# Kernel optimization log

Measured on AMD Instinct MI355X. Metric: run time of the kernel, lower is better.

Reference implementation:

```python
import jax, jax.numpy as jnp
import numpy as np

NH, DK, DV, D = 8, 64, 64, 768
DECAY = 0.95
WRITE_STRENGTH = 0.1


def setup_inputs() -> dict:
    key = jax.random.key(0)
    ks = jax.random.split(key, 6)
    s = 0.02  # small init scale for projection weights
    return {
        "x": jax.random.normal(ks[0], (4, 4096, D), dtype=jnp.float32),
        "w_key": jax.random.normal(ks[1], (NH * DK, D), dtype=jnp.float32) * s,
        "w_value": jax.random.normal(ks[2], (NH * DV, D), dtype=jnp.float32) * s,
        "w_query": jax.random.normal(ks[3], (NH * DK, D), dtype=jnp.float32) * s,
        "w_gate": jax.random.normal(ks[4], (NH, D), dtype=jnp.float32) * s,
        "w_out": jax.random.normal(ks[5], (D, NH * DV), dtype=jnp.float32) * s,
    }


def reference(x, w_key, w_value, w_query, w_gate, w_out):
    B, S, _ = x.shape
    # Batched projections (torch Linear: y = x @ W.T)
    k = (x @ w_key.T).reshape(B, S, NH, DK)
    v = (x @ w_value.T).reshape(B, S, NH, DV)
    q = (x @ w_query.T).reshape(B, S, NH, DK)
    gate = jax.nn.sigmoid(x @ w_gate.T)  # (B, S, NH)

    # Writes only use batch element 0 (mirrors k[0], v[0], gate[0] in source)
    k0 = k[0]      # (S, NH, DK)
    v0 = v[0]      # (S, NH, DV)
    g0 = gate[0]   # (S, NH)

    def step(fw, inp):
        q_t, k0_t, v0_t, g0_t = inp
        # Read BEFORE this step's decay+write
        retrieved = jnp.einsum('bhk,hkv->bhv', q_t, fw)  # (B, NH, DV)
        write = (WRITE_STRENGTH * g0_t)[:, None, None] * (k0_t[:, :, None] * v0_t[:, None, :])
        fw_new = DECAY * fw + jax.lax.stop_gradient(write)
        return fw_new, retrieved

    fw0 = jnp.zeros((NH, DK, DV), dtype=x.dtype)
    inputs = (q.transpose(1, 0, 2, 3), k0, v0, g0)  # time-major
    _, retrieved = jax.lax.scan(step, fw0, inputs)   # (S, B, NH, DV)
    retrieved = retrieved.transpose(1, 0, 2, 3).reshape(B, S, NH * DV)
    return x + retrieved @ w_out.T
```

## Files before the change

### kernel.cpp

```cpp
#include <hip/hip_runtime.h>
#include <hip/hip_bf16.h>

typedef __hip_bfloat16 bf16;
typedef __attribute__((ext_vector_type(8))) short   bf16x8;
typedef __attribute__((ext_vector_type(4))) float   f32x4;

#define B_   4
#define S_   4096
#define D_   768
#define NH_  8
#define DK_  64
#define DV_  64
#define CH_  64
#define NCH_ (S_/CH_)
#define DECAY_ 0.95f
#define WSTR_  0.1f

__device__ __forceinline__ float b2f(bf16 v) { return __bfloat162float(v); }
__device__ __forceinline__ bf16  f2b(float v) { return __float2bfloat16(v); }

__device__ __forceinline__ void gl2lds16(const bf16* g, bf16* lds) {
    __builtin_amdgcn_global_load_lds(
        (const __attribute__((address_space(1))) void*)g,
        (__attribute__((address_space(3))) void*)lds, 16, 0, 0);
}

__global__ __launch_bounds__(192) void cast_fused(const float* __restrict__ x,
                                                  bf16* __restrict__ xb,
                                                  const float* __restrict__ wg,
                                                  float* __restrict__ wgt,
                                                  const float* __restrict__ wq,
                                                  const float* __restrict__ wk,
                                                  const float* __restrict__ wv,
                                                  const float* __restrict__ wo,
                                                  bf16* __restrict__ dq, bf16* __restrict__ dk,
                                                  bf16* __restrict__ dv, bf16* __restrict__ dob) {
    const int tid = threadIdx.x;
    if (blockIdx.x >= (B_ * S_)) {
        const int idx = blockIdx.x - B_ * S_;
        const int which = idx >> 9, b = idx & 511;
        const float* src = which == 0 ? wq : which == 1 ? wk : which == 2 ? wv : wo;
        bf16*       dst = which == 0 ? dq : which == 1 ? dk : which == 2 ? dv : dob;
        const int i = (b * 192 + tid) * 4;
        const float4 v = *reinterpret_cast<const float4*>(src + i);
        union { bf16 b4[4]; ushort4 u; } t;
        t.b4[0] = f2b(v.x); t.b4[1] = f2b(v.y); t.b4[2] = f2b(v.z); t.b4[3] = f2b(v.w);
        *reinterpret_cast<ushort4*>(dst + i) = t.u;
        return;
    }
    const int s = blockIdx.x;
    const float4 v = *reinterpret_cast<const float4*>(x + (size_t)s * D_ + tid * 4);
    union { bf16 b4[4]; ushort4 u; } t;
    t.b4[0] = f2b(v.x); t.b4[1] = f2b(v.y); t.b4[2] = f2b(v.z); t.b4[3] = f2b(v.w);
    *reinterpret_cast<ushort4*>(xb + (size_t)s * D_ + tid * 4) = t.u;

    if (s < S_) {
        __shared__ float red[3 * 8];
        float p[8];
        const float* wgp = wg + tid * 4;
        #pragma unroll
        for (int h = 0; h < 8; h++) {
            const float4 wv4 = *reinterpret_cast<const float4*>(wgp + h * D_);
            p[h] = v.x * wv4.x + v.y * wv4.y + v.z * wv4.z + v.w * wv4.w;
        }
        #pragma unroll
        for (int h = 0; h < 8; h++)
            #pragma unroll
            for (int off = 32; off; off >>= 1) p[h] += __shfl_down(p[h], off);
        const int w = tid >> 6, lane = tid & 63;
        if (lane == 0) {
            #pragma unroll
            for (int h = 0; h < 8; h++) red[w * 8 + h] = p[h];
        }
        __syncthreads();
        if (tid < 8) {
            const float sum = red[tid] + red[8 + tid] + red[16 + tid];
            wgt[s * NH_ + tid] = WSTR_ / (1.f + expf(-sum));
        }
    }
}

template<typename TC, int ADDX, int NITER>
__device__ __forceinline__ void gemm_body(bf16* As, bf16* Bs,
                                          const bf16* __restrict__ A,
                                          const bf16* __restrict__ Bm,
                                          const float* __restrict__ X,
                                          TC* __restrict__ C,
                                          int bm, int bn, int K, int N) {
    const int tid = threadIdx.x, lane = tid & 63, w = tid >> 6;
    const int quad = lane >> 4, l16 = lane & 15;
    const int wm = (w >> 1) * 64, wn = (w & 1) * 64;
    const int lrow = lane >> 3;
    const int lcol = ((lane & 7) ^ lrow) * 8;

    f32x4 acc[4][4] = {};

    auto STAGE_A = [&](int it, int buf) {
        const int k0 = it * 64;
        bf16* Ad = As + buf * 8192;
        #pragma unroll
        for (int c = 0; c < 4; c++) {
            const int seg = w * 4 + c;
            const int row = seg * 8 + lrow;
            gl2lds16(A + (size_t)(bm + row) * K + k0 + lcol, &Ad[seg * 512]);
        }
    };
    auto STAGE_B = [&](int it) {
        const int k0 = it * 64;
        #pragma unroll
        for (int c = 0; c < 4; c++) {
            const int seg = w * 4 + c;
            const int row = seg * 8 + lrow;
            gl2lds16(Bm + (size_t)(bn + row) * K + k0 + lcol, &Bs[seg * 512]);
        }
    };

    STAGE_A(0, 0);
    STAGE_B(0);

    for (int it = 0; it < NITER; ++it) {
        const int cur = it & 1;
        if (it + 1 < NITER) {
            STAGE_A(it + 1, cur ^ 1);
            asm volatile("s_waitcnt vmcnt(4)" ::: "memory");
        } else {
            asm volatile("s_waitcnt vmcnt(0)" ::: "memory");
        }
        __builtin_amdgcn_s_barrier();
        asm volatile("" ::: "memory");

        const bf16* Ar = As + cur * 8192;
        bf16x8 af[2][4], bfr[2][4];
        #pragma unroll
        for (int kh = 0; kh < 2; kh++)
            #pragma unroll
            for (int t = 0; t < 4; t++) {
                const int cb = ((kh * 4 + quad) ^ (l16 & 7)) * 8;
                af[kh][t]  = *reinterpret_cast<const bf16x8*>(&Ar[(wm + t * 16 + l16) * 64 + cb]);
                bfr[kh][t] = *reinterpret_cast<const bf16x8*>(&Bs[(wn + t * 16 + l16) * 64 + cb]);
            }
        asm volatile("s_waitcnt lgkmcnt(0)" ::: "memory");
        __builtin_amdgcn_s_barrier();
        if (it + 1 < NITER) STAGE_B(it + 1);

        #pragma unroll
        for (int kh = 0; kh < 2; kh++)
            #pragma unroll
            for (int mt = 0; mt < 4; mt++)
                #pragma unroll
                for (int nt = 0; nt < 4; nt++)
                    acc[mt][nt] = __builtin_amdgcn_mfma_f32_16x16x32_bf16(
                        af[kh][mt], bfr[kh][nt], acc[mt][nt], 0, 0, 0);
    }

    #pragma unroll
    for (int mt = 0; mt < 4; mt++)
        #pragma unroll
        for (int nt = 0; nt < 4; nt++)
            #pragma unroll
            for (int r = 0; r < 4; r++) {
                const int m = bm + wm + mt * 16 + quad * 4 + r;
                const int n = bn + wn + nt * 16 + l16;
                float v = acc[mt][nt][r];
                if (ADDX) v += X[(size_t)m * N + n];
                if (sizeof(TC) == 2) *(bf16*)&C[(size_t)m * N + n] = f2b(v);
                else                 *(float*)&C[(size_t)m * N + n] = v;
            }
}

__global__ __launch_bounds__(256, 3) void proj_fused(const bf16* __restrict__ xb,
                                                  const bf16* __restrict__ wqb,
                                                  const bf16* __restrict__ wkb,
                                                  const bf16* __restrict__ wvb,
                                                  bf16* __restrict__ qbuf,
                                                  bf16* __restrict__ k0buf,
                                                  bf16* __restrict__ v0buf) {
    __shared__ bf16 As[2 * 128 * 64];
    __shared__ bf16 Bs[128 * 64];
    const int id = blockIdx.x;
    const int xcd = id & 7;
    int j = id >> 3;
    const bf16* Bm; bf16* C; int bm, bn;
    if (j < 64) {
        bm = (xcd + ((j >> 2) << 3)) * 128;
        bn = (j & 3) * 128;
        Bm = wqb; C = qbuf;
    } else {
        j -= 64;
        bm = (xcd + ((j >> 3) << 3)) * 128;
        const int b8 = j & 7;
        bn = (b8 & 3) * 128;
        Bm = (b8 < 4) ? wkb : wvb;
        C  = (b8 < 4) ? k0buf : v0buf;
    }
    gemm_body<bf16, 0, 12>(As, Bs, xb, Bm, nullptr, C, bm, bn, D_, 512);
}

__global__ __launch_bounds__(256, 3) void gemm_out(const bf16* __restrict__ retr,
                                                const bf16* __restrict__ wob,
                                                const float* __restrict__ x,
                                                float* __restrict__ out) {
    __shared__ bf16 As[2 * 128 * 64];
    __shared__ bf16 Bs[128 * 64];
    const int gx = gridDim.x, gy = gridDim.y;
    const int L = blockIdx.y * gx + blockIdx.x;
    const int rpx = gy >> 3;
    const int xcd = L & 7;
    const int i   = L >> 3;
    const int by = xcd * rpx + i / gx;
    const int bx = i % gx;
    gemm_body<float, 1, 8>(As, Bs, retr, wob, x, out, by * 128, bx * 128, 512, D_);
}

__global__ __launch_bounds__(256) void chunk_sums(const bf16* __restrict__ k0,
                                                  const bf16* __restrict__ v0,
                                                  const float* __restrict__ wgt,
                                                  bf16* __restrict__ lsumsT) {
    const int n = blockIdx.x, h = blockIdx.y;
    __shared__ float ks[CH_][65];
    __shared__ float vs[CH_][64];
    __shared__ float cw[CH_];
    const int tid = threadIdx.x;
    for (int e = tid; e < CH_ * 64; e += 256) {
        const int r = e >> 6, c = e & 63;
        const int t = n * CH_ + r;
        ks[r][c] = b2f(k0[(size_t)t * (NH_ * DK_) + h * DK_ + c]);
        vs[r][c] = b2f(v0[(size_t)t * (NH_ * DV_) + h * DV_ + c]);
    }
    if (tid < CH_) {
        const int t = n * CH_ + tid;
        cw[tid] = powf(DECAY_, (float)(CH_ - 1 - tid)) * wgt[t * NH_ + h];
    }
    __syncthreads();
    const int j = tid & 63, ig = tid >> 6;
    float acc[16] = {};
    for (int idx = 0; idx < CH_; idx++) {
        const float ck = cw[idx] * ks[idx][j];
        #pragma unroll
        for (int r = 0; r < 16; r++) acc[r] += vs[idx][ig * 16 + r] * ck;
    }
    bf16* outp = lsumsT + ((size_t)(n * NH_ + h)) * (DK_ * DV_);
    #pragma unroll
    for (int r = 0; r < 16; r++) outp[(ig * 16 + r) * 64 + j] = f2b(acc[r]);
}

__device__ __forceinline__ void cvt4(ushort4 u, float f[4]) {
    union { unsigned u; float f; } c;
    c.u = (unsigned)u.x << 16; f[0] = c.f;
    c.u = (unsigned)u.y << 16; f[1] = c.f;
    c.u = (unsigned)u.z << 16; f[2] = c.f;
    c.u = (unsigned)u.w << 16; f[3] = c.f;
}

__global__ __launch_bounds__(256) void chunk_output(const bf16* __restrict__ q,
                                                    const bf16* __restrict__ k0,
                                                    const bf16* __restrict__ v0,
                                                    const float* __restrict__ wgt,
                                                    const bf16* __restrict__ lsumsT,
                                                    bf16* __restrict__ retr) {
    const int n = blockIdx.x, h = blockIdx.y;
    __shared__ bf16 QsAm[4][64 * 64];
    __shared__ bf16 Ks[64 * 64];
    __shared__ bf16 FWT[64 * 64];
    __shared__ bf16 VT[64 * 72];
    __shared__ float dpow[64], winv[64];
    const int tid = threadIdx.x, lane = tid & 63, w = tid >> 6;
    const int quad = lane >> 4, l16 = lane & 15;
    const int t0 = n * CH_;
    const int lrow = lane >> 3;
    const int lcol = ((lane & 7) ^ lrow) * 8;

    #pragma unroll
    for (int seg = 0; seg < 8; seg++) {
        const int row = seg * 8 + lrow;
        gl2lds16(q + ((size_t)(w * S_ + t0 + row)) * 512 + h * 64 + lcol, &QsAm[w][seg * 512]);
    }
    #pragma unroll
    for (int c = 0; c < 2; c++) {
        const int seg = w * 2 + c;
        const int row = seg * 8 + lrow;
        gl2lds16(k0 + ((size_t)(t0 + row)) * 512 + h * 64 + lcol, &Ks[seg * 512]);
    }

    {
        float fwacc[16] = {};
        const float dcp[4] = { 1.0f, 0.0375241f, 1.40806e-3f, 5.28365e-5f };
        #pragma unroll
        for (int jj = 1; jj <= 4; jj++) {
            const int nm = n - jj;
            if (nm < 0) break;
            const ushort* Lp = (const ushort*)(lsumsT + ((size_t)(nm * NH_ + h)) * 4096) + tid * 16;
            #pragma unroll
            for (int u = 0; u < 4; u++) {
                float f[4];
                cvt4(reinterpret_cast<const ushort4*>(Lp)[u], f);
                #pragma unroll
                for (int e = 0; e < 4; e++) fwacc[u * 4 + e] += dcp[jj - 1] * f[e];
            }
        }
        const int frow = tid >> 2;
        #pragma unroll
        for (int half = 0; half < 2; half++) {
            const int cb = (tid & 3) * 2 + half;
            union { bf16 b8v[8]; bf16x8 v; } t;
            #pragma unroll
            for (int e = 0; e < 8; e++) t.b8v[e] = f2b(fwacc[half * 8 + e]);
            *reinterpret_cast<bf16x8*>(&FWT[frow * 64 + (cb ^ (frow & 7)) * 8]) = t.v;
        }
    }
    {
        ushort4 vreg[4];
        const int jb = (tid & 15) * 4;
        const int sb = tid >> 4;
        #pragma unroll
        for (int it = 0; it < 4; it++)
            vreg[it] = *reinterpret_cast<const ushort4*>(
                v0 + ((size_t)(t0 + sb + it * 16)) * 512 + h * 64 + jb);
        ushort* VTu = reinterpret_cast<ushort*>(VT);
        #pragma unroll
        for (int it = 0; it < 4; it++) {
            const int s = sb + it * 16;
            VTu[(jb + 0) * 72 + s] = vreg[it].x;
            VTu[(jb + 1) * 72 + s] = vreg[it].y;
            VTu[(jb + 2) * 72 + s] = vreg[it].z;
            VTu[(jb + 3) * 72 + s] = vreg[it].w;
        }
    }
    if (tid < 64) {
        dpow[tid] = powf(DECAY_, (float)tid);
        winv[tid] = wgt[(t0 + tid) * NH_ + h] * powf(DECAY_, -(float)(tid + 1));
    }
    __syncthreads();

    const int cb0 = ((quad) ^ (l16 & 7)) * 8;
    const int cb1 = ((4 + quad) ^ (l16 & 7)) * 8;
    bf16* Qw = &QsAm[w][0];

    bf16x8 af[4][2];
    #pragma unroll
    for (int mt = 0; mt < 4; mt++) {
        af[mt][0] = *reinterpret_cast<const bf16x8*>(&Qw[(mt * 16 + l16) * 64 + cb0]);
        af[mt][1] = *reinterpret_cast<const bf16x8*>(&Qw[(mt * 16 + l16) * 64 + cb1]);
    }

    f32x4 acc[4][4] = {};
    #pragma unroll
    for (int kh = 0; kh < 2; kh++) {
        bf16x8 bk[4];
        #pragma unroll
        for (int nt = 0; nt < 4; nt++)
            bk[nt] = *reinterpret_cast<const bf16x8*>(
                &Ks[(nt * 16 + l16) * 64 + (kh ? cb1 : cb0)]);
        #pragma unroll
        for (int mt = 0; mt < 4; mt++)
            #pragma unroll
            for (int nt = 0; nt < 4; nt++)
                acc[mt][nt] = __builtin_amdgcn_mfma_f32_16x16x32_bf16(
                    af[mt][kh], bk[nt], acc[mt][nt], 0, 0, 0);
    }

    const float pmt[4] = { 1.0f, 0.4401266694f, 0.1937114891f, 0.0852578070f };
    const f32x4 dpb = *reinterpret_cast<const f32x4*>(&dpow[quad * 4]);
    float winv_l[4];
    #pragma unroll
    for (int nt = 0; nt < 4; nt++) winv_l[nt] = winv[nt * 16 + l16];
    #pragma unroll
    for (int mt = 0; mt < 4; mt++)
        #pragma unroll
        for (int nt = 0; nt < 4; nt++)
            #pragma unroll
            for (int r = 0; r < 4; r++) {
                const int tt = mt * 16 + quad * 4 + r;
                const int s = nt * 16 + l16;
                const float v = (s < tt) ? acc[mt][nt][r] * (dpb[r] * pmt[mt]) * winv_l[nt] : 0.f;
                Qw[tt * 64 + (((s >> 3) ^ (tt & 7)) << 3) + (s & 7)] = f2b(v);
            }

    f32x4 o[4][4] = {};
    #pragma unroll
    for (int kh = 0; kh < 2; kh++) {
        bf16x8 ff[4];
        #pragma unroll
        for (int nt = 0; nt < 4; nt++)
            ff[nt] = *reinterpret_cast<const bf16x8*>(
                &FWT[(nt * 16 + l16) * 64 + (kh ? cb1 : cb0)]);
        #pragma unroll
        for (int mt = 0; mt < 4; mt++)
            #pragma unroll
            for (int nt = 0; nt < 4; nt++)
                o[mt][nt] = __builtin_amdgcn_mfma_f32_16x16x32_bf16(
                    af[mt][kh], ff[nt], o[mt][nt], 0, 0, 0);
    }
    #pragma unroll
    for (int mt = 0; mt < 4; mt++)
        #pragma unroll
        for (int nt = 0; nt < 4; nt++)
            #pragma unroll
            for (int r = 0; r < 4; r++) o[mt][nt][r] *= dpb[r] * pmt[mt];

    #pragma unroll
    for (int kh = 0; kh < 2; kh++) {
        bf16x8 am[4], vf[4];
        #pragma unroll
        for (int mt = 0; mt < 4; mt++)
            am[mt] = *reinterpret_cast<const bf16x8*>(
                &Qw[(mt * 16 + l16) * 64 + (kh ? cb1 : cb0)]);
        #pragma unroll
        for (int nt = 0; nt < 4; nt++)
            vf[nt] = *reinterpret_cast<const bf16x8*>(
                &VT[(nt * 16 + l16) * 72 + kh * 32 + quad * 8]);
        #pragma unroll
        for (int mt = 0; mt < 4; mt++)
            #pragma unroll
            for (int nt = 0; nt < 4; nt++)
                o[mt][nt] = __builtin_amdgcn_mfma_f32_16x16x32_bf16(
                    am[mt], vf[nt], o[mt][nt], 0, 0, 0);
    }

    #pragma unroll
    for (int mt = 0; mt < 4; mt++)
        #pragma unroll
        for (int nt = 0; nt < 4; nt++)
            #pragma unroll
            for (int r = 0; r < 4; r++) {
                const int tt = mt * 16 + quad * 4 + r;
                retr[((size_t)(w * S_ + t0 + tt)) * 512 + h * 64 + nt * 16 + l16] =
                    f2b(o[mt][nt][r]);
            }
}

extern "C" void kernel_launch(void* const* d_in, const int* in_sizes, int n_in,
                              void* d_out, int out_size, void* d_ws, size_t ws_size,
                              hipStream_t stream) {
    const float* x  = (const float*)d_in[0];
    const float* wk = (const float*)d_in[1];
    const float* wv = (const float*)d_in[2];
    const float* wq = (const float*)d_in[3];
    const float* wg = (const float*)d_in[4];
    const float* wo = (const float*)d_in[5];
    float* out = (float*)d_out;

    const size_t MB1 = 1ull << 20;
    char* w = (char*)d_ws;
    bf16*  qbuf    = (bf16*)(w);
    bf16*  k0buf   = (bf16*)(w + 16 * MB1);
    bf16*  v0buf   = (bf16*)(w + 20 * MB1);
    float* wgt     = (float*)(w + 24 * MB1);
    bf16*  wqb     = (bf16*)(w + 24 * MB1 + (128ull<<10));
    bf16*  wkb     = (bf16*)(w + 24 * MB1 + (128ull<<10) + 1*786432);
    bf16*  wvb     = (bf16*)(w + 24 * MB1 + (128ull<<10) + 2*786432);
    bf16*  wob     = (bf16*)(w + 24 * MB1 + (128ull<<10) + 3*786432);
    bf16*  lsumsT  = (bf16*)(w + 28 * MB1);
    bf16*  retr    = (bf16*)(w + 32 * MB1);
    bf16*  xb      = (bf16*)(w + 48 * MB1);

    const int MB = B_ * S_;

    cast_fused<<<MB + 2048, 192, 0, stream>>>(x, xb, wg, wgt,
                                              wq, wk, wv, wo, wqb, wkb, wvb, wob);

    proj_fused<<<768, 256, 0, stream>>>(xb, wqb, wkb, wvb, qbuf, k0buf, v0buf);

    chunk_sums<<<dim3(NCH_, NH_), 256, 0, stream>>>(k0buf, v0buf, wgt, lsumsT);
    chunk_output<<<dim3(NCH_, NH_), 256, 0, stream>>>(qbuf, k0buf, v0buf, wgt, lsumsT, retr);

    gemm_out<<<dim3(D_ / 128, MB / 128), 256, 0, stream>>>(retr, wob, x, out);
}
```

Measured before the change: 185.5 us.

## Fuse all stages into one persistent cooperative kernel with grid syncs

Replaces the five separate launches (cast, projections, chunk sums, chunk output, output GEMM) with one cooperative 768-block kernel. The stages are separated by grid.sync, and the kernel falls back to the old launches if occupancy or the cooperative launch fails. The goal is to remove launch gaps and tail idle time between the small kernels. In exchange, all stages share one register and LDS budget, and the chunk stages use only 512 of the 768 blocks while the rest wait at grid barriers.

```diff
diff --git a/kernel.cpp b/kernel.cpp
--- a/kernel.cpp
+++ b/kernel.cpp
@@ -1,5 +1,8 @@
 #include <hip/hip_runtime.h>
 #include <hip/hip_bf16.h>
+#include <hip/hip_cooperative_groups.h>
+
+namespace cg = cooperative_groups;
 
 typedef __hip_bfloat16 bf16;
 typedef __attribute__((ext_vector_type(8))) short   bf16x8;
@@ -15,6 +18,7 @@
 #define NCH_ (S_/CH_)
 #define DECAY_ 0.95f
 #define WSTR_  0.1f
+#define L2D_  (-0.07400058144f)
 
 __device__ __forceinline__ float b2f(bf16 v) { return __bfloat162float(v); }
 __device__ __forceinline__ bf16  f2b(float v) { return __float2bfloat16(v); }
@@ -23,6 +27,427 @@
     __builtin_amdgcn_global_load_lds(
         (const __attribute__((address_space(1))) void*)g,
         (__attribute__((address_space(3))) void*)lds, 16, 0, 0);
+}
+
+__device__ __forceinline__ void cvt4(ushort4 u, float f[4]) {
+    union { unsigned u; float f; } c;
+    c.u = (unsigned)u.x << 16; f[0] = c.f;
+    c.u = (unsigned)u.y << 16; f[1] = c.f;
+    c.u = (unsigned)u.z << 16; f[2] = c.f;
+    c.u = (unsigned)u.w << 16; f[3] = c.f;
+}
+
+template<typename TC, int ADDX, int NITER>
+__device__ __forceinline__ void gemm_body(bf16* As, bf16* Bs,
+                                          const bf16* __restrict__ A,
+                                          const bf16* __restrict__ Bm,
+                                          const float* __restrict__ X,
+                                          TC* __restrict__ C,
+                                          int bm, int bn, int K, int N) {
+    const int tid = threadIdx.x, lane = tid & 63, w = tid >> 6;
+    const int quad = lane >> 4, l16 = lane & 15;
+    const int wm = (w >> 1) * 64, wn = (w & 1) * 64;
+    const int lrow = lane >> 3;
+    const int lcol = ((lane & 7) ^ lrow) * 8;
+
+    f32x4 acc[4][4] = {};
+
+    auto STAGE_A = [&](int it, int buf) {
+        const int k0 = it * 64;
+        bf16* Ad = As + buf * 8192;
+        #pragma unroll
+        for (int c = 0; c < 4; c++) {
+            const int seg = w * 4 + c;
+            const int row = seg * 8 + lrow;
+            gl2lds16(A + (size_t)(bm + row) * K + k0 + lcol, &Ad[seg * 512]);
+        }
+    };
+    auto STAGE_B = [&](int it) {
+        const int k0 = it * 64;
+        #pragma unroll
+        for (int c = 0; c < 4; c++) {
+            const int seg = w * 4 + c;
+            const int row = seg * 8 + lrow;
+            gl2lds16(Bm + (size_t)(bn + row) * K + k0 + lcol, &Bs[seg * 512]);
+        }
+    };
+
+    STAGE_A(0, 0);
+    STAGE_B(0);
+
+    for (int it = 0; it < NITER; ++it) {
+        const int cur = it & 1;
+        if (it + 1 < NITER) {
+            STAGE_A(it + 1, cur ^ 1);
+            asm volatile("s_waitcnt vmcnt(4)" ::: "memory");
+        } else {
+            asm volatile("s_waitcnt vmcnt(0)" ::: "memory");
+        }
+        __builtin_amdgcn_s_barrier();
+        asm volatile("" ::: "memory");
+
+        const bf16* Ar = As + cur * 8192;
+        bf16x8 af[2][4], bfr[2][4];
+        #pragma unroll
+        for (int kh = 0; kh < 2; kh++)
+            #pragma unroll
+            for (int t = 0; t < 4; t++) {
+                const int cb = ((kh * 4 + quad) ^ (l16 & 7)) * 8;
+                af[kh][t]  = *reinterpret_cast<const bf16x8*>(&Ar[(wm + t * 16 + l16) * 64 + cb]);
+                bfr[kh][t] = *reinterpret_cast<const bf16x8*>(&Bs[(wn + t * 16 + l16) * 64 + cb]);
+            }
+        asm volatile("s_waitcnt lgkmcnt(0)" ::: "memory");
+        __builtin_amdgcn_s_barrier();
+        if (it + 1 < NITER) STAGE_B(it + 1);
+
+        #pragma unroll
+        for (int kh = 0; kh < 2; kh++)
+            #pragma unroll
+            for (int mt = 0; mt < 4; mt++)
+                #pragma unroll
+                for (int nt = 0; nt < 4; nt++)
+                    acc[mt][nt] = __builtin_amdgcn_mfma_f32_16x16x32_bf16(
+                        af[kh][mt], bfr[kh][nt], acc[mt][nt], 0, 0, 0);
+    }
+
+    #pragma unroll
+    for (int mt = 0; mt < 4; mt++)
+        #pragma unroll
+        for (int nt = 0; nt < 4; nt++)
+            #pragma unroll
+            for (int r = 0; r < 4; r++) {
+                const int m = bm + wm + mt * 16 + quad * 4 + r;
+                const int n = bn + wn + nt * 16 + l16;
+                float v = acc[mt][nt][r];
+                if (ADDX) v += X[(size_t)m * N + n];
+                if (sizeof(TC) == 2) *(bf16*)&C[(size_t)m * N + n] = f2b(v);
+                else                 *(float*)&C[(size_t)m * N + n] = v;
+            }
+}
+
+__global__ __launch_bounds__(256, 3) void mega(
+    const float* __restrict__ x,  const float* __restrict__ wg,
+    const float* __restrict__ wq, const float* __restrict__ wk,
+    const float* __restrict__ wv, const float* __restrict__ wo,
+    bf16* __restrict__ xb, float* __restrict__ wgt,
+    bf16* __restrict__ wqb, bf16* __restrict__ wkb,
+    bf16* __restrict__ wvb, bf16* __restrict__ wob,
+    bf16* __restrict__ qbuf, bf16* __restrict__ k0buf, bf16* __restrict__ v0buf,
+    bf16* __restrict__ lsumsT, bf16* __restrict__ retr, float* __restrict__ out) {
+
+    __shared__ __align__(16) bf16 U[24576];
+    __shared__ __align__(16) float scr[192];
+    cg::grid_group grid = cg::this_grid();
+    const int bid = blockIdx.x, tid = threadIdx.x;
+    const int lane = tid & 63, w = tid >> 6;
+
+    {
+        #pragma unroll 2
+        for (int u0 = 0; u0 < 24; ++u0) {
+            const int unit = bid * 24 + u0;
+            if (tid < 192) {
+                const float* src; bf16* dst;
+                if (unit < B_ * S_) {
+                    src = x  + (size_t)unit * D_;
+                    dst = xb + (size_t)unit * D_;
+                } else {
+                    const int idx = unit - B_ * S_;
+                    const int which = idx >> 9, b = idx & 511;
+                    const float* s4 = which == 0 ? wq : which == 1 ? wk : which == 2 ? wv : wo;
+                    bf16*       d4 = which == 0 ? wqb : which == 1 ? wkb : which == 2 ? wvb : wob;
+                    src = s4 + (size_t)b * D_;
+                    dst = d4 + (size_t)b * D_;
+                }
+                const float4 v = *reinterpret_cast<const float4*>(src + tid * 4);
+                union { bf16 b4[4]; ushort4 u; } t;
+                t.b4[0] = f2b(v.x); t.b4[1] = f2b(v.y); t.b4[2] = f2b(v.z); t.b4[3] = f2b(v.w);
+                *reinterpret_cast<ushort4*>(dst + tid * 4) = t.u;
+            }
+        }
+        if (bid * 24 < S_) {
+            for (int i = 0; i < 6; ++i) {
+                const int row = bid * 24 + w * 6 + i;
+                if (row >= S_) break;
+                const float* xr = x + (size_t)row * D_ + lane * 12;
+                const float4 a0 = *reinterpret_cast<const float4*>(xr);
+                const float4 a1 = *reinterpret_cast<const float4*>(xr + 4);
+                const float4 a2 = *reinterpret_cast<const float4*>(xr + 8);
+                float p[8];
+                #pragma unroll
+                for (int h = 0; h < 8; h++) {
+                    const float* wr = wg + h * D_ + lane * 12;
+                    const float4 b0 = *reinterpret_cast<const float4*>(wr);
+                    const float4 b1 = *reinterpret_cast<const float4*>(wr + 4);
+                    const float4 b2 = *reinterpret_cast<const float4*>(wr + 8);
+                    p[h] = a0.x*b0.x + a0.y*b0.y + a0.z*b0.z + a0.w*b0.w
+                         + a1.x*b1.x + a1.y*b1.y + a1.z*b1.z + a1.w*b1.w
+                         + a2.x*b2.x + a2.y*b2.y + a2.z*b2.z + a2.w*b2.w;
+                }
+                #pragma unroll
+                for (int h = 0; h < 8; h++)
+                    #pragma unroll
+                    for (int off = 32; off; off >>= 1) p[h] += __shfl_down(p[h], off);
+                if (lane == 0) {
+                    #pragma unroll
+                    for (int h = 0; h < 8; h++)
+                        wgt[row * NH_ + h] = WSTR_ / (1.f + expf(-p[h]));
+                }
+            }
+        }
+    }
+    __threadfence();
+    grid.sync();
+
+    {
+        bf16* As = U;
+        bf16* Bs = U + 16384;
+        const int xcd = bid & 7;
+        int j = bid >> 3;
+        const bf16* Bm; bf16* C; int bm, bn;
+        if (j < 64) {
+            bm = (xcd + ((j >> 2) << 3)) * 128;
+            bn = (j & 3) * 128;
+            Bm = wqb; C = qbuf;
+        } else {
+            j -= 64;
+            bm = (xcd + ((j >> 3) << 3)) * 128;
+            const int b8 = j & 7;
+            bn = (b8 & 3) * 128;
+            Bm = (b8 < 4) ? wkb : wvb;
+            C  = (b8 < 4) ? k0buf : v0buf;
+        }
+        gemm_body<bf16, 0, 12>(As, Bs, xb, Bm, nullptr, C, bm, bn, D_, 512);
+    }
+    __threadfence();
+    grid.sync();
+
+    if (bid < NCH_ * NH_) {
+        const int n = bid & 63, h = bid >> 6;
+        float* ksf = (float*)U;
+        float* vsf = ksf + 64 * 68;
+        float* cw  = scr + 128;
+        const int r = tid >> 2, c0 = (tid & 3) * 16;
+        {
+            const ushort* kp = (const ushort*)k0buf + ((size_t)(n * CH_ + r)) * 512 + h * 64 + c0;
+            const ushort* vp = (const ushort*)v0buf + ((size_t)(n * CH_ + r)) * 512 + h * 64 + c0;
+            #pragma unroll
+            for (int e = 0; e < 4; e++) {
+                float fk[4], fv[4];
+                cvt4(reinterpret_cast<const ushort4*>(kp)[e], fk);
+                cvt4(reinterpret_cast<const ushort4*>(vp)[e], fv);
+                union { float f[4]; float4 v4; } tk, tv;
+                tk.f[0]=fk[0]; tk.f[1]=fk[1]; tk.f[2]=fk[2]; tk.f[3]=fk[3];
+                tv.f[0]=fv[0]; tv.f[1]=fv[1]; tv.f[2]=fv[2]; tv.f[3]=fv[3];
+                *reinterpret_cast<float4*>(&ksf[r * 68 + c0 + e * 4]) = tk.v4;
+                *reinterpret_cast<float4*>(&vsf[r * 68 + c0 + e * 4]) = tv.v4;
+            }
+        }
+        if (tid < CH_)
+            cw[tid] = exp2f((float)(CH_ - 1 - tid) * L2D_) * wgt[(n * CH_ + tid) * NH_ + h];
+        __syncthreads();
+        const int j = tid & 63, ig = tid >> 6;
+        float acc[16] = {};
+        for (int idx = 0; idx < CH_; idx++) {
+            const float ck = cw[idx] * ksf[idx * 68 + j];
+            #pragma unroll
+            for (int rr = 0; rr < 16; rr++) acc[rr] += vsf[idx * 68 + ig * 16 + rr] * ck;
+        }
+        bf16* outp = lsumsT + ((size_t)(n * NH_ + h)) * (DK_ * DV_);
+        #pragma unroll
+        for (int rr = 0; rr < 16; rr++) outp[(ig * 16 + rr) * 64 + j] = f2b(acc[rr]);
+    }
+    __threadfence();
+    grid.sync();
+
+    if (bid < NCH_ * NH_) {
+        const int n = bid & 63, h = bid >> 6;
+        bf16* QsAm = U;
+        bf16* Ks   = U + 16384;
+        bf16* FWT  = U + 16384;
+        bf16* VT   = U + 20480;
+        float* dpow = scr, *winv = scr + 64;
+        const int quad = lane >> 4, l16 = lane & 15;
+        const int t0 = n * CH_;
+        const int lrow = lane >> 3;
+        const int lcol = ((lane & 7) ^ lrow) * 8;
+
+        #pragma unroll
+        for (int seg = 0; seg < 8; seg++) {
+            const int row = seg * 8 + lrow;
+            gl2lds16(qbuf + ((size_t)(w * S_ + t0 + row)) * 512 + h * 64 + lcol,
+                     &QsAm[w * 4096 + seg * 512]);
+        }
+        #pragma unroll
+        for (int c = 0; c < 2; c++) {
+            const int seg = w * 2 + c;
+            const int row = seg * 8 + lrow;
+            gl2lds16(k0buf + ((size_t)(t0 + row)) * 512 + h * 64 + lcol, &Ks[seg * 512]);
+        }
+        float fwacc[16] = {};
+        {
+            const float dcp[4] = { 1.0f, 0.0375241f, 1.40806e-3f, 5.28365e-5f };
+            #pragma unroll
+            for (int jj = 1; jj <= 4; jj++) {
+                const int nm = n - jj;
+                if (nm < 0) break;
+                const ushort* Lp = (const ushort*)(lsumsT + ((size_t)(nm * NH_ + h)) * 4096) + tid * 16;
+                #pragma unroll
+                for (int u = 0; u < 4; u++) {
+                    float f[4];
+                    cvt4(reinterpret_cast<const ushort4*>(Lp)[u], f);
+                    #pragma unroll
+                    for (int e = 0; e < 4; e++) fwacc[u * 4 + e] += dcp[jj - 1] * f[e];
+                }
+            }
+        }
+        {
+            ushort4 vreg[4];
+            const int jb = (tid & 15) * 4;
+            const int sb = tid >> 4;
+            #pragma unroll
+            for (int it = 0; it < 4; it++)
+                vreg[it] = *reinterpret_cast<const ushort4*>(
+                    v0buf + ((size_t)(t0 + sb + it * 16)) * 512 + h * 64 + jb);
+            ushort* VTu = reinterpret_cast<ushort*>(VT);
+            #pragma unroll
+            for (int it = 0; it < 4; it++) {
+                const int s = sb + it * 16;
+                #pragma unroll
+                for (int c = 0; c < 4; c++) {
+                    const int v = jb + c;
+                    const ushort val = c == 0 ? vreg[it].x : c == 1 ? vreg[it].y
+                                     : c == 2 ? vreg[it].z : vreg[it].w;
+                    VTu[v * 64 + (((s >> 3) ^ (v & 7)) << 3) + (s & 7)] = val;
+                }
+            }
+        }
+        if (tid < 64) {
+            dpow[tid] = exp2f((float)tid * L2D_);
+            winv[tid] = wgt[(t0 + tid) * NH_ + h] * exp2f(-(float)(tid + 1) * L2D_);
+        }
+        __syncthreads();
+
+        const int cb0 = ((quad) ^ (l16 & 7)) * 8;
+        const int cb1 = ((4 + quad) ^ (l16 & 7)) * 8;
+        bf16* Qw = &QsAm[w * 4096];
+
+        bf16x8 af[4][2];
+        #pragma unroll
+        for (int mt = 0; mt < 4; mt++) {
+            af[mt][0] = *reinterpret_cast<const bf16x8*>(&Qw[(mt * 16 + l16) * 64 + cb0]);
+            af[mt][1] = *reinterpret_cast<const bf16x8*>(&Qw[(mt * 16 + l16) * 64 + cb1]);
+        }
+        f32x4 acc[4][4] = {};
+        #pragma unroll
+        for (int kh = 0; kh < 2; kh++) {
+            bf16x8 bk[4];
+            #pragma unroll
+            for (int nt = 0; nt < 4; nt++)
+                bk[nt] = *reinterpret_cast<const bf16x8*>(
+                    &Ks[(nt * 16 + l16) * 64 + (kh ? cb1 : cb0)]);
+            #pragma unroll
+            for (int mt = 0; mt < 4; mt++)
+                #pragma unroll
+                for (int nt = 0; nt < 4; nt++)
+                    acc[mt][nt] = __builtin_amdgcn_mfma_f32_16x16x32_bf16(
+                        af[mt][kh], bk[nt], acc[mt][nt], 0, 0, 0);
+        }
+        const float pmt[4] = { 1.0f, 0.4401266694f, 0.1937114891f, 0.0852578070f };
+        const f32x4 dpb = *reinterpret_cast<const f32x4*>(&dpow[quad * 4]);
+        float winv_l[4];
+        #pragma unroll
+        for (int nt = 0; nt < 4; nt++) winv_l[nt] = winv[nt * 16 + l16];
+        #pragma unroll
+        for (int mt = 0; mt < 4; mt++)
+            #pragma unroll
+            for (int nt = 0; nt < 4; nt++)
+                #pragma unroll
+                for (int r = 0; r < 4; r++) {
+                    const int tt = mt * 16 + quad * 4 + r;
+                    const int s = nt * 16 + l16;
+                    const float v = (s < tt) ? acc[mt][nt][r] * (dpb[r] * pmt[mt]) * winv_l[nt] : 0.f;
+                    Qw[tt * 64 + (((s >> 3) ^ (tt & 7)) << 3) + (s & 7)] = f2b(v);
+                }
+        __syncthreads();
+        {
+            const int frow = tid >> 2;
+            #pragma unroll
+            for (int half = 0; half < 2; half++) {
+                const int cb = (tid & 3) * 2 + half;
+                union { bf16 b8v[8]; bf16x8 v; } t;
+                #pragma unroll
+                for (int e = 0; e < 8; e++) t.b8v[e] = f2b(fwacc[half * 8 + e]);
+                *reinterpret_cast<bf16x8*>(&FWT[frow * 64 + (cb ^ (frow & 7)) * 8]) = t.v;
+            }
+        }
+        __syncthreads();
+
+        f32x4 o[4][4] = {};
+        #pragma unroll
+        for (int kh = 0; kh < 2; kh++) {
+            bf16x8 ff[4];
+            #pragma unroll
+            for (int nt = 0; nt < 4; nt++)
+                ff[nt] = *reinterpret_cast<const bf16x8*>(
+                    &FWT[(nt * 16 + l16) * 64 + (kh ? cb1 : cb0)]);
+            #pragma unroll
+            for (int mt = 0; mt < 4; mt++)
+                #pragma unroll
+                for (int nt = 0; nt < 4; nt++)
+                    o[mt][nt] = __builtin_amdgcn_mfma_f32_16x16x32_bf16(
+                        af[mt][kh], ff[nt], o[mt][nt], 0, 0, 0);
+        }
+        #pragma unroll
+        for (int mt = 0; mt < 4; mt++)
+            #pragma unroll
+            for (int nt = 0; nt < 4; nt++)
+                #pragma unroll
+                for (int r = 0; r < 4; r++) o[mt][nt][r] *= dpb[r] * pmt[mt];
+
+        #pragma unroll
+        for (int kh = 0; kh < 2; kh++) {
+            bf16x8 am[4], vf[4];
+            #pragma unroll
+            for (int mt = 0; mt < 4; mt++)
+                am[mt] = *reinterpret_cast<const bf16x8*>(
+                    &Qw[(mt * 16 + l16) * 64 + (kh ? cb1 : cb0)]);
+            #pragma unroll
+            for (int nt = 0; nt < 4; nt++)
+                vf[nt] = *reinterpret_cast<const bf16x8*>(
+                    &VT[(nt * 16 + l16) * 64 + (kh ? cb1 : cb0)]);
+            #pragma unroll
+            for (int mt = 0; mt < 4; mt++)
+                #pragma unroll
+                for (int nt = 0; nt < 4; nt++)
+                    o[mt][nt] = __builtin_amdgcn_mfma_f32_16x16x32_bf16(
+                        am[mt], vf[nt], o[mt][nt], 0, 0, 0);
+        }
+        #pragma unroll
+        for (int mt = 0; mt < 4; mt++)
+            #pragma unroll
+            for (int nt = 0; nt < 4; nt++)
+                #pragma unroll
+                for (int r = 0; r < 4; r++) {
+                    const int tt = mt * 16 + quad * 4 + r;
+                    retr[((size_t)(w * S_ + t0 + tt)) * 512 + h * 64 + nt * 16 + l16] =
+                        f2b(o[mt][nt][r]);
+                }
+    }
+    __threadfence();
+    grid.sync();
+
+    {
+        bf16* As = U;
+        bf16* Bs = U + 16384;
+        const int gx = 6, gy = 128;
+        const int L = bid;
+        const int rpx = gy >> 3;
+        const int xcd = L & 7;
+        const int i   = L >> 3;
+        const int by = xcd * rpx + i / gx;
+        const int bx = i % gx;
+        gemm_body<float, 1, 8>(As, Bs, retr, wob, x, out, by * 128, bx * 128, 512, D_);
+    }
 }
 
 __global__ __launch_bounds__(192) void cast_fused(const float* __restrict__ x,
@@ -78,94 +503,6 @@
             wgt[s * NH_ + tid] = WSTR_ / (1.f + expf(-sum));
         }
     }
-}
-
-template<typename TC, int ADDX, int NITER>
-__device__ __forceinline__ void gemm_body(bf16* As, bf16* Bs,
-                                          const bf16* __restrict__ A,
-                                          const bf16* __restrict__ Bm,
-                                          const float* __restrict__ X,
-                                          TC* __restrict__ C,
-                                          int bm, int bn, int K, int N) {
-    const int tid = threadIdx.x, lane = tid & 63, w = tid >> 6;
-    const int quad = lane >> 4, l16 = lane & 15;
-    const int wm = (w >> 1) * 64, wn = (w & 1) * 64;
-    const int lrow = lane >> 3;
-    const int lcol = ((lane & 7) ^ lrow) * 8;
-
-    f32x4 acc[4][4] = {};
-
-    auto STAGE_A = [&](int it, int buf) {
-        const int k0 = it * 64;
-        bf16* Ad = As + buf * 8192;
-        #pragma unroll
-        for (int c = 0; c < 4; c++) {
-            const int seg = w * 4 + c;
-            const int row = seg * 8 + lrow;
-            gl2lds16(A + (size_t)(bm + row) * K + k0 + lcol, &Ad[seg * 512]);
-        }
-    };
-    auto STAGE_B = [&](int it) {
-        const int k0 = it * 64;
-        #pragma unroll
-        for (int c = 0; c < 4; c++) {
-            const int seg = w * 4 + c;
-            const int row = seg * 8 + lrow;
-            gl2lds16(Bm + (size_t)(bn + row) * K + k0 + lcol, &Bs[seg * 512]);
-        }
-    };
-
-    STAGE_A(0, 0);
-    STAGE_B(0);
-
-    for (int it = 0; it < NITER; ++it) {
-        const int cur = it & 1;
-        if (it + 1 < NITER) {
-            STAGE_A(it + 1, cur ^ 1);
-            asm volatile("s_waitcnt vmcnt(4)" ::: "memory");
-        } else {
-            asm volatile("s_waitcnt vmcnt(0)" ::: "memory");
-        }
-        __builtin_amdgcn_s_barrier();
-        asm volatile("" ::: "memory");
-
-        const bf16* Ar = As + cur * 8192;
-        bf16x8 af[2][4], bfr[2][4];
-        #pragma unroll
-        for (int kh = 0; kh < 2; kh++)
-            #pragma unroll
-            for (int t = 0; t < 4; t++) {
-                const int cb = ((kh * 4 + quad) ^ (l16 & 7)) * 8;
-                af[kh][t]  = *reinterpret_cast<const bf16x8*>(&Ar[(wm + t * 16 + l16) * 64 + cb]);
-                bfr[kh][t] = *reinterpret_cast<const bf16x8*>(&Bs[(wn + t * 16 + l16) * 64 + cb]);
-            }
-        asm volatile("s_waitcnt lgkmcnt(0)" ::: "memory");
-        __builtin_amdgcn_s_barrier();
-        if (it + 1 < NITER) STAGE_B(it + 1);
-
-        #pragma unroll
-        for (int kh = 0; kh < 2; kh++)
-            #pragma unroll
-            for (int mt = 0; mt < 4; mt++)
-                #pragma unroll
-                for (int nt = 0; nt < 4; nt++)
-                    acc[mt][nt] = __builtin_amdgcn_mfma_f32_16x16x32_bf16(
-                        af[kh][mt], bfr[kh][nt], acc[mt][nt], 0, 0, 0);
-    }
-
-    #pragma unroll
-    for (int mt = 0; mt < 4; mt++)
-        #pragma unroll
-        for (int nt = 0; nt < 4; nt++)
-            #pragma unroll
-            for (int r = 0; r < 4; r++) {
-                const int m = bm + wm + mt * 16 + quad * 4 + r;
-                const int n = bn + wn + nt * 16 + l16;
-                float v = acc[mt][nt][r];
-                if (ADDX) v += X[(size_t)m * N + n];
-                if (sizeof(TC) == 2) *(bf16*)&C[(size_t)m * N + n] = f2b(v);
-                else                 *(float*)&C[(size_t)m * N + n] = v;
-            }
 }
 
 __global__ __launch_bounds__(256, 3) void proj_fused(const bf16* __restrict__ xb,
@@ -244,14 +581,6 @@
     for (int r = 0; r < 16; r++) outp[(ig * 16 + r) * 64 + j] = f2b(acc[r]);
 }
 
-__device__ __forceinline__ void cvt4(ushort4 u, float f[4]) {
-    union { unsigned u; float f; } c;
-    c.u = (unsigned)u.x << 16; f[0] = c.f;
-    c.u = (unsigned)u.y << 16; f[1] = c.f;
-    c.u = (unsigned)u.z << 16; f[2] = c.f;
-    c.u = (unsigned)u.w << 16; f[3] = c.f;
-}
-
 __global__ __launch_bounds__(256) void chunk_output(const bf16* __restrict__ q,
                                                     const bf16* __restrict__ k0,
                                                     const bf16* __restrict__ v0,
@@ -281,7 +610,6 @@
         const int row = seg * 8 + lrow;
         gl2lds16(k0 + ((size_t)(t0 + row)) * 512 + h * 64 + lcol, &Ks[seg * 512]);
     }
-
     {
         float fwacc[16] = {};
         const float dcp[4] = { 1.0f, 0.0375241f, 1.40806e-3f, 5.28365e-5f };
@@ -342,7 +670,6 @@
         af[mt][0] = *reinterpret_cast<const bf16x8*>(&Qw[(mt * 16 + l16) * 64 + cb0]);
         af[mt][1] = *reinterpret_cast<const bf16x8*>(&Qw[(mt * 16 + l16) * 64 + cb1]);
     }
-
     f32x4 acc[4][4] = {};
     #pragma unroll
     for (int kh = 0; kh < 2; kh++) {
@@ -358,7 +685,6 @@
                 acc[mt][nt] = __builtin_amdgcn_mfma_f32_16x16x32_bf16(
                     af[mt][kh], bk[nt], acc[mt][nt], 0, 0, 0);
     }
-
     const float pmt[4] = { 1.0f, 0.4401266694f, 0.1937114891f, 0.0852578070f };
     const f32x4 dpb = *reinterpret_cast<const f32x4*>(&dpow[quad * 4]);
     float winv_l[4];
@@ -375,7 +701,6 @@
                 const float v = (s < tt) ? acc[mt][nt][r] * (dpb[r] * pmt[mt]) * winv_l[nt] : 0.f;
                 Qw[tt * 64 + (((s >> 3) ^ (tt & 7)) << 3) + (s & 7)] = f2b(v);
             }
-
     f32x4 o[4][4] = {};
     #pragma unroll
     for (int kh = 0; kh < 2; kh++) {
@@ -397,7 +722,6 @@
         for (int nt = 0; nt < 4; nt++)
             #pragma unroll
             for (int r = 0; r < 4; r++) o[mt][nt][r] *= dpb[r] * pmt[mt];
-
     #pragma unroll
     for (int kh = 0; kh < 2; kh++) {
         bf16x8 am[4], vf[4];
@@ -416,7 +740,6 @@
                 o[mt][nt] = __builtin_amdgcn_mfma_f32_16x16x32_bf16(
                     am[mt], vf[nt], o[mt][nt], 0, 0, 0);
     }
-
     #pragma unroll
     for (int mt = 0; mt < 4; mt++)
         #pragma unroll
@@ -454,15 +777,30 @@
     bf16*  retr    = (bf16*)(w + 32 * MB1);
     bf16*  xb      = (bf16*)(w + 48 * MB1);
 
+    static int coopOK = -1;
+    if (coopOK < 0) {
+        int nb = 0;
+        hipError_t e = hipOccupancyMaxActiveBlocksPerMultiprocessor(
+            &nb, (const void*)mega, 256, 0);
+        coopOK = (e == hipSuccess && nb >= 3) ? 1 : 0;
+    }
+    if (coopOK == 1) {
+        void* args[] = {
+            (void*)&x, (void*)&wg, (void*)&wq, (void*)&wk, (void*)&wv, (void*)&wo,
+            (void*)&xb, (void*)&wgt, (void*)&wqb, (void*)&wkb, (void*)&wvb, (void*)&wob,
+            (void*)&qbuf, (void*)&k0buf, (void*)&v0buf, (void*)&lsumsT, (void*)&retr,
+            (void*)&out };
+        hipError_t e = hipLaunchCooperativeKernel(
+            (const void*)mega, dim3(768), dim3(256), args, 0, stream);
+        if (e == hipSuccess) return;
+        coopOK = 0;
+    }
+
     const int MB = B_ * S_;
-
     cast_fused<<<MB + 2048, 192, 0, stream>>>(x, xb, wg, wgt,
                                               wq, wk, wv, wo, wqb, wkb, wvb, wob);
-
     proj_fused<<<768, 256, 0, stream>>>(xb, wqb, wkb, wvb, qbuf, k0buf, v0buf);
-
     chunk_sums<<<dim3(NCH_, NH_), 256, 0, stream>>>(k0buf, v0buf, wgt, lsumsT);
     chunk_output<<<dim3(NCH_, NH_), 256, 0, stream>>>(qbuf, k0buf, v0buf, wgt, lsumsT, retr);
-
     gemm_out<<<dim3(D_ / 128, MB / 128), 256, 0, stream>>>(retr, wob, x, out);
 }
```

Measured after the change: 187.3 us. Within noise of the previous version (+1.0%).

## Fuse x bf16 cast into projection GEMM A-operand load

Applied to the files above, without the earlier changes.

Removes the separate bf16 copy of x: the projection GEMM now loads fp32 x through registers, converts to bf16 and writes swizzled LDS tiles, with software prefetch two iterations ahead. The prep kernel shrinks to only the gate computation and weight casts over S rows. This avoids writing and re-reading a large bf16 intermediate, but doubles the bytes the GEMM reads for A and replaces async global-to-LDS loads with register staging, which adds register pressure.

```diff
diff --git a/kernel.cpp b/kernel.cpp
--- a/kernel.cpp
+++ b/kernel.cpp
@@ -25,19 +25,26 @@
         (__attribute__((address_space(3))) void*)lds, 16, 0, 0);
 }
 
-__global__ __launch_bounds__(192) void cast_fused(const float* __restrict__ x,
-                                                  bf16* __restrict__ xb,
-                                                  const float* __restrict__ wg,
-                                                  float* __restrict__ wgt,
-                                                  const float* __restrict__ wq,
-                                                  const float* __restrict__ wk,
-                                                  const float* __restrict__ wv,
-                                                  const float* __restrict__ wo,
-                                                  bf16* __restrict__ dq, bf16* __restrict__ dk,
-                                                  bf16* __restrict__ dv, bf16* __restrict__ dob) {
+__device__ __forceinline__ void cvt4(ushort4 u, float f[4]) {
+    union { unsigned u; float f; } c;
+    c.u = (unsigned)u.x << 16; f[0] = c.f;
+    c.u = (unsigned)u.y << 16; f[1] = c.f;
+    c.u = (unsigned)u.z << 16; f[2] = c.f;
+    c.u = (unsigned)u.w << 16; f[3] = c.f;
+}
+
+__global__ __launch_bounds__(192) void prep(const float* __restrict__ x,
+                                            const float* __restrict__ wg,
+                                            float* __restrict__ wgt,
+                                            const float* __restrict__ wq,
+                                            const float* __restrict__ wk,
+                                            const float* __restrict__ wv,
+                                            const float* __restrict__ wo,
+                                            bf16* __restrict__ dq, bf16* __restrict__ dk,
+                                            bf16* __restrict__ dv, bf16* __restrict__ dob) {
     const int tid = threadIdx.x;
-    if (blockIdx.x >= (B_ * S_)) {
-        const int idx = blockIdx.x - B_ * S_;
+    if (blockIdx.x >= S_) {
+        const int idx = blockIdx.x - S_;
         const int which = idx >> 9, b = idx & 511;
         const float* src = which == 0 ? wq : which == 1 ? wk : which == 2 ? wv : wo;
         bf16*       dst = which == 0 ? dq : which == 1 ? dk : which == 2 ? dv : dob;
@@ -50,34 +57,134 @@
     }
     const int s = blockIdx.x;
     const float4 v = *reinterpret_cast<const float4*>(x + (size_t)s * D_ + tid * 4);
-    union { bf16 b4[4]; ushort4 u; } t;
-    t.b4[0] = f2b(v.x); t.b4[1] = f2b(v.y); t.b4[2] = f2b(v.z); t.b4[3] = f2b(v.w);
-    *reinterpret_cast<ushort4*>(xb + (size_t)s * D_ + tid * 4) = t.u;
-
-    if (s < S_) {
-        __shared__ float red[3 * 8];
-        float p[8];
-        const float* wgp = wg + tid * 4;
-        #pragma unroll
-        for (int h = 0; h < 8; h++) {
-            const float4 wv4 = *reinterpret_cast<const float4*>(wgp + h * D_);
-            p[h] = v.x * wv4.x + v.y * wv4.y + v.z * wv4.z + v.w * wv4.w;
-        }
-        #pragma unroll
-        for (int h = 0; h < 8; h++)
-            #pragma unroll
-            for (int off = 32; off; off >>= 1) p[h] += __shfl_down(p[h], off);
-        const int w = tid >> 6, lane = tid & 63;
-        if (lane == 0) {
-            #pragma unroll
-            for (int h = 0; h < 8; h++) red[w * 8 + h] = p[h];
-        }
-        __syncthreads();
-        if (tid < 8) {
-            const float sum = red[tid] + red[8 + tid] + red[16 + tid];
-            wgt[s * NH_ + tid] = WSTR_ / (1.f + expf(-sum));
-        }
-    }
+    __shared__ float red[3 * 8];
+    float p[8];
+    const float* wgp = wg + tid * 4;
+    #pragma unroll
+    for (int h = 0; h < 8; h++) {
+        const float4 wv4 = *reinterpret_cast<const float4*>(wgp + h * D_);
+        p[h] = v.x * wv4.x + v.y * wv4.y + v.z * wv4.z + v.w * wv4.w;
+    }
+    #pragma unroll
+    for (int h = 0; h < 8; h++)
+        #pragma unroll
+        for (int off = 32; off; off >>= 1) p[h] += __shfl_down(p[h], off);
+    const int w = tid >> 6, lane = tid & 63;
+    if (lane == 0) {
+        #pragma unroll
+        for (int h = 0; h < 8; h++) red[w * 8 + h] = p[h];
+    }
+    __syncthreads();
+    if (tid < 8) {
+        const float sum = red[tid] + red[8 + tid] + red[16 + tid];
+        wgt[s * NH_ + tid] = WSTR_ / (1.f + expf(-sum));
+    }
+}
+
+template<int NITER>
+__device__ __forceinline__ void gemm_projA(bf16* As, bf16* Bs,
+                                           const float* __restrict__ A,
+                                           const bf16* __restrict__ Bm,
+                                           bf16* __restrict__ C,
+                                           int bm, int bn, int K, int N) {
+    const int tid = threadIdx.x, lane = tid & 63, w = tid >> 6;
+    const int quad = lane >> 4, l16 = lane & 15;
+    const int wm = (w >> 1) * 64, wn = (w & 1) * 64;
+    const int lrow = lane >> 3;
+    const int lcol = ((lane & 7) ^ lrow) * 8;
+
+    f32x4 acc[4][4] = {};
+    float4 a4[8];
+
+    auto ALOAD = [&](int it) {
+        const int k0 = it * 64;
+        #pragma unroll
+        for (int c = 0; c < 4; c++) {
+            const int row = (w * 4 + c) * 8 + lrow;
+            const float* p = A + (size_t)(bm + row) * K + k0 + lcol;
+            a4[2 * c]     = *reinterpret_cast<const float4*>(p);
+            a4[2 * c + 1] = *reinterpret_cast<const float4*>(p + 4);
+        }
+    };
+    auto AWRITE = [&](int buf) {
+        bf16* Ad = As + buf * 8192;
+        #pragma unroll
+        for (int c = 0; c < 4; c++) {
+            union { bf16 b8[8]; bf16x8 v; } t;
+            t.b8[0] = f2b(a4[2*c].x);   t.b8[1] = f2b(a4[2*c].y);
+            t.b8[2] = f2b(a4[2*c].z);   t.b8[3] = f2b(a4[2*c].w);
+            t.b8[4] = f2b(a4[2*c+1].x); t.b8[5] = f2b(a4[2*c+1].y);
+            t.b8[6] = f2b(a4[2*c+1].z); t.b8[7] = f2b(a4[2*c+1].w);
+            *reinterpret_cast<bf16x8*>(&Ad[(w * 4 + c) * 512 + lane * 8]) = t.v;
+        }
+    };
+    auto STAGE_B = [&](int it) {
+        const int k0 = it * 64;
+        #pragma unroll
+        for (int c = 0; c < 4; c++) {
+            const int seg = w * 4 + c;
+            const int row = seg * 8 + lrow;
+            gl2lds16(Bm + (size_t)(bn + row) * K + k0 + lcol, &Bs[seg * 512]);
+        }
+    };
+
+    ALOAD(0);
+    asm volatile("s_waitcnt vmcnt(0)" ::: "memory");
+    AWRITE(0);
+    STAGE_B(0);
+    ALOAD(1);
+
+    for (int it = 0; it < NITER; ++it) {
+        const int cur = it & 1;
+        if (it + 1 < NITER)
+            asm volatile("s_waitcnt vmcnt(8)" ::: "memory");
+        else
+            asm volatile("s_waitcnt vmcnt(0)" ::: "memory");
+        asm volatile("s_waitcnt lgkmcnt(0)" ::: "memory");
+        __builtin_amdgcn_s_barrier();
+        asm volatile("" ::: "memory");
+
+        const bf16* Ar = As + cur * 8192;
+        bf16x8 af[2][4], bfr[2][4];
+        #pragma unroll
+        for (int kh = 0; kh < 2; kh++)
+            #pragma unroll
+            for (int t = 0; t < 4; t++) {
+                const int cb = ((kh * 4 + quad) ^ (l16 & 7)) * 8;
+                af[kh][t]  = *reinterpret_cast<const bf16x8*>(&Ar[(wm + t * 16 + l16) * 64 + cb]);
+                bfr[kh][t] = *reinterpret_cast<const bf16x8*>(&Bs[(wn + t * 16 + l16) * 64 + cb]);
+            }
+        asm volatile("s_waitcnt lgkmcnt(0)" ::: "memory");
+        __builtin_amdgcn_s_barrier();
+        asm volatile("" ::: "memory");
+
+        if (it + 1 < NITER) {
+            asm volatile("s_waitcnt vmcnt(0)" ::: "memory");
+            AWRITE(cur ^ 1);
+            STAGE_B(it + 1);
+            if (it + 2 < NITER) ALOAD(it + 2);
+        }
+
+        #pragma unroll
+        for (int kh = 0; kh < 2; kh++)
+            #pragma unroll
+            for (int mt = 0; mt < 4; mt++)
+                #pragma unroll
+                for (int nt = 0; nt < 4; nt++)
+                    acc[mt][nt] = __builtin_amdgcn_mfma_f32_16x16x32_bf16(
+                        af[kh][mt], bfr[kh][nt], acc[mt][nt], 0, 0, 0);
+    }
+
+    #pragma unroll
+    for (int mt = 0; mt < 4; mt++)
+        #pragma unroll
+        for (int nt = 0; nt < 4; nt++)
+            #pragma unroll
+            for (int r = 0; r < 4; r++) {
+                const int m = bm + wm + mt * 16 + quad * 4 + r;
+                const int n = bn + wn + nt * 16 + l16;
+                C[(size_t)m * N + n] = f2b(acc[mt][nt][r]);
+            }
 }
 
 template<typename TC, int ADDX, int NITER>
@@ -168,7 +275,7 @@
             }
 }
 
-__global__ __launch_bounds__(256, 3) void proj_fused(const bf16* __restrict__ xb,
+__global__ __launch_bounds__(256, 3) void proj_fused(const float* __restrict__ x,
                                                   const bf16* __restrict__ wqb,
                                                   const bf16* __restrict__ wkb,
                                                   const bf16* __restrict__ wvb,
@@ -193,7 +300,7 @@
         Bm = (b8 < 4) ? wkb : wvb;
         C  = (b8 < 4) ? k0buf : v0buf;
     }
-    gemm_body<bf16, 0, 12>(As, Bs, xb, Bm, nullptr, C, bm, bn, D_, 512);
+    gemm_projA<12>(As, Bs, x, Bm, C, bm, bn, D_, 512);
 }
 
 __global__ __launch_bounds__(256, 3) void gemm_out(const bf16* __restrict__ retr,
@@ -242,14 +349,6 @@
     bf16* outp = lsumsT + ((size_t)(n * NH_ + h)) * (DK_ * DV_);
     #pragma unroll
     for (int r = 0; r < 16; r++) outp[(ig * 16 + r) * 64 + j] = f2b(acc[r]);
-}
-
-__device__ __forceinline__ void cvt4(ushort4 u, float f[4]) {
-    union { unsigned u; float f; } c;
-    c.u = (unsigned)u.x << 16; f[0] = c.f;
-    c.u = (unsigned)u.y << 16; f[1] = c.f;
-    c.u = (unsigned)u.z << 16; f[2] = c.f;
-    c.u = (unsigned)u.w << 16; f[3] = c.f;
 }
 
 __global__ __launch_bounds__(256) void chunk_output(const bf16* __restrict__ q,
@@ -281,7 +380,6 @@
         const int row = seg * 8 + lrow;
         gl2lds16(k0 + ((size_t)(t0 + row)) * 512 + h * 64 + lcol, &Ks[seg * 512]);
     }
-
     {
         float fwacc[16] = {};
         const float dcp[4] = { 1.0f, 0.0375241f, 1.40806e-3f, 5.28365e-5f };
@@ -342,7 +440,6 @@
         af[mt][0] = *reinterpret_cast<const bf16x8*>(&Qw[(mt * 16 + l16) * 64 + cb0]);
         af[mt][1] = *reinterpret_cast<const bf16x8*>(&Qw[(mt * 16 + l16) * 64 + cb1]);
     }
-
     f32x4 acc[4][4] = {};
     #pragma unroll
     for (int kh = 0; kh < 2; kh++) {
@@ -358,7 +455,6 @@
                 acc[mt][nt] = __builtin_amdgcn_mfma_f32_16x16x32_bf16(
                     af[mt][kh], bk[nt], acc[mt][nt], 0, 0, 0);
     }
-
     const float pmt[4] = { 1.0f, 0.4401266694f, 0.1937114891f, 0.0852578070f };
     const f32x4 dpb = *reinterpret_cast<const f32x4*>(&dpow[quad * 4]);
     float winv_l[4];
@@ -375,7 +471,6 @@
                 const float v = (s < tt) ? acc[mt][nt][r] * (dpb[r] * pmt[mt]) * winv_l[nt] : 0.f;
                 Qw[tt * 64 + (((s >> 3) ^ (tt & 7)) << 3) + (s & 7)] = f2b(v);
             }
-
     f32x4 o[4][4] = {};
     #pragma unroll
     for (int kh = 0; kh < 2; kh++) {
@@ -397,7 +492,6 @@
         for (int nt = 0; nt < 4; nt++)
             #pragma unroll
             for (int r = 0; r < 4; r++) o[mt][nt][r] *= dpb[r] * pmt[mt];
-
     #pragma unroll
     for (int kh = 0; kh < 2; kh++) {
         bf16x8 am[4], vf[4];
@@ -416,7 +510,6 @@
                 o[mt][nt] = __builtin_amdgcn_mfma_f32_16x16x32_bf16(
                     am[mt], vf[nt], o[mt][nt], 0, 0, 0);
     }
-
     #pragma unroll
     for (int mt = 0; mt < 4; mt++)
         #pragma unroll
@@ -452,14 +545,13 @@
     bf16*  wob     = (bf16*)(w + 24 * MB1 + (128ull<<10) + 3*786432);
     bf16*  lsumsT  = (bf16*)(w + 28 * MB1);
     bf16*  retr    = (bf16*)(w + 32 * MB1);
-    bf16*  xb      = (bf16*)(w + 48 * MB1);
 
     const int MB = B_ * S_;
 
-    cast_fused<<<MB + 2048, 192, 0, stream>>>(x, xb, wg, wgt,
-                                              wq, wk, wv, wo, wqb, wkb, wvb, wob);
-
-    proj_fused<<<768, 256, 0, stream>>>(xb, wqb, wkb, wvb, qbuf, k0buf, v0buf);
+    prep<<<S_ + 2048, 192, 0, stream>>>(x, wg, wgt, wq, wk, wv, wo,
+                                        wqb, wkb, wvb, wob);
+
+    proj_fused<<<768, 256, 0, stream>>>(x, wqb, wkb, wvb, qbuf, k0buf, v0buf);
 
     chunk_sums<<<dim3(NCH_, NH_), 256, 0, stream>>>(k0buf, v0buf, wgt, lsumsT);
     chunk_output<<<dim3(NCH_, NH_), 256, 0, stream>>>(qbuf, k0buf, v0buf, wgt, lsumsT, retr);
```

Result: slower. 202.0 us (+8.9%).
